# Kernel optimization log

Hardware: AMD Instinct MI355X
Metric: run time of the kernel (lower is better)

Reference implementation:

```python
import math
import jax, jax.numpy as jnp
import numpy as np

D_MODEL = 1024
N_HEAD = 16
HEAD_DIM = D_MODEL // N_HEAD
THETA = 10000.0


def precompute_rope(seq_len, head_dim):
    half = head_dim // 2
    inv_freq = 1.0 / (THETA ** (jnp.arange(half, dtype=jnp.float32) / half))
    pos = jnp.arange(seq_len, dtype=jnp.float32)
    freqs = jnp.outer(pos, inv_freq)  # [S, half]
    return jnp.cos(freqs), jnp.sin(freqs)


def apply_rope(x, cos, sin):
    # x: [B, H, S, Dh]; cos/sin: [S, Dh//2] -> broadcast over B, H
    x_even = x[..., 0::2]
    x_odd = x[..., 1::2]
    cos = cos[None, None]
    sin = sin[None, None]
    out_even = x_even * cos - x_odd * sin
    out_odd = x_even * sin + x_odd * cos
    # interleave back: stack on last axis then flatten pairs
    return jnp.stack((out_even, out_odd), axis=-1).reshape(x.shape)


def setup_inputs() -> dict:
    key = jax.random.key(0)
    kx, kq, kp = jax.random.split(key, 3)
    x = jax.random.normal(kx, (4, 2048, D_MODEL), dtype=jnp.float32)
    s = 1.0 / math.sqrt(D_MODEL)
    # torch Linear weight is [out, in]; we store transposed [in, out] for x @ W
    W_qkv = jax.random.normal(kq, (D_MODEL, 3 * D_MODEL), dtype=jnp.float32) * s
    W_proj = jax.random.normal(kp, (D_MODEL, D_MODEL), dtype=jnp.float32) * s
    return {"x": x, "W_qkv": W_qkv, "W_proj": W_proj}


def reference(x, W_qkv, W_proj):
    bsz, seqlen, d_model = x.shape
    qkv = x @ W_qkv  # [B, S, 3D]
    q, k, v = jnp.split(qkv, 3, axis=-1)
    def to_heads(t):
        return t.reshape(bsz, seqlen, N_HEAD, HEAD_DIM).transpose(0, 2, 1, 3)
    q, k, v = to_heads(q), to_heads(k), to_heads(v)  # [B, H, S, Dh]
    cos, sin = precompute_rope(seqlen, HEAD_DIM)
    q = apply_rope(q, cos, sin)
    k = apply_rope(k, cos, sin)
    att = jnp.einsum('bhqd,bhkd->bhqk', q, k) * (1.0 / math.sqrt(HEAD_DIM))
    causal = jnp.tril(jnp.ones((seqlen, seqlen), dtype=bool))
    att = jnp.where(causal[None, None], att, -jnp.inf)
    att = jax.nn.softmax(att, axis=-1)
    y = jnp.einsum('bhqk,bhkd->bhqd', att, v)
    y = y.transpose(0, 2, 1, 3).reshape(bsz, seqlen, d_model)
    return y @ W_proj
```

## Files before the change

### kernel.cpp

```cpp
#include <hip/hip_runtime.h>


#define BATCH 4
#define SEQ   2048
#define DM    1024
#define NH    16
#define HD    64
#define QKV_W 3072

typedef short bf16x8 __attribute__((ext_vector_type(8)));
typedef float f32x4  __attribute__((ext_vector_type(4)));
typedef unsigned short bf16_t;

__device__ __forceinline__ unsigned short f2bf(float f) {
  unsigned u = __float_as_uint(f);
  u += 0x7fffu + ((u >> 16) & 1u);
  return (unsigned short)(u >> 16);
}
__device__ __forceinline__ float bf2f(unsigned short s) {
  return __uint_as_float((unsigned)s << 16);
}
__device__ __forceinline__ void gld16(const void* g, void* l) {
  __builtin_amdgcn_global_load_lds(
      (const __attribute__((address_space(1))) unsigned int*)g,
      (__attribute__((address_space(3))) unsigned int*)l, 16, 0, 0);
}

__global__ __launch_bounds__(256) void k_transpose(const float* __restrict__ W,
                                                   bf16_t* __restrict__ Wt,
                                                   int K, int N) {
  __shared__ float tile[32][33];
  const int tx = threadIdx.x, ty = threadIdx.y;
  const int n0 = blockIdx.x * 32, k0 = blockIdx.y * 32;
#pragma unroll
  for (int j = 0; j < 4; ++j)
    tile[ty + j * 8][tx] = W[(size_t)(k0 + ty + j * 8) * N + n0 + tx];
  __syncthreads();
#pragma unroll
  for (int j = 0; j < 4; ++j)
    Wt[(size_t)(n0 + ty + j * 8) * K + k0 + tx] = f2bf(tile[tx][ty + j * 8]);
}

__global__ __launch_bounds__(256) void k_cvt(const float* __restrict__ x,
                                             bf16_t* __restrict__ xb) {
  const int i = (blockIdx.x * 256 + threadIdx.x) * 4;
  float4 v = *(const float4*)(x + i);
  unsigned lo = (unsigned)f2bf(v.x) | ((unsigned)f2bf(v.y) << 16);
  unsigned hi = (unsigned)f2bf(v.z) | ((unsigned)f2bf(v.w) << 16);
  *(uint2*)(xb + i) = make_uint2(lo, hi);
}

__global__ __launch_bounds__(256) void k_rope(bf16_t* __restrict__ qkv) {
  const int t = blockIdx.x * 256 + threadIdx.x;
  const int i = t & 31;
  const int h = (t >> 5) & 15;
  const int s = (t >> 9) & 2047;
  const int b = t >> 20;
  const float inv = __expf((float)i * -0.28782313662425575f);
  float sn, cs;
  sincosf((float)s * inv, &sn, &cs);
  size_t base = ((size_t)(b * SEQ + s)) * QKV_W + h * HD + 2 * i;
#pragma unroll
  for (int part = 0; part < 2; ++part) {
    unsigned u = *(unsigned*)(qkv + base + part * DM);
    float e = bf2f((unsigned short)(u & 0xffffu));
    float o = bf2f((unsigned short)(u >> 16));
    unsigned short e2 = f2bf(e * cs - o * sn);
    unsigned short o2 = f2bf(e * sn + o * cs);
    *(unsigned*)(qkv + base + part * DM) = (unsigned)e2 | ((unsigned)o2 << 16);
  }
}

template<int MODE>
__global__ __launch_bounds__(256) void k_gemm(const bf16_t* __restrict__ A,
                                              const bf16_t* __restrict__ Bt,
                                              void* __restrict__ Cout,
                                              bf16_t* __restrict__ vt,
                                              int M, int N, int K) {
  __shared__ __align__(16) short As[128 * 32];
  __shared__ __align__(16) short Bs[128 * 32];
  const int tid = threadIdx.x;
  const int wave = tid >> 6, lane = tid & 63;
  const int quad = lane >> 4, l16 = lane & 15;
  const int wm = (wave >> 1) * 64, wn = (wave & 1) * 64;
  const int bm = blockIdx.y * 128, bn = blockIdx.x * 128;

  f32x4 acc[4][4];
#pragma unroll
  for (int i = 0; i < 4; ++i)
#pragma unroll
    for (int j = 0; j < 4; ++j) acc[i][j] = f32x4{0.f, 0.f, 0.f, 0.f};

  const int r0 = tid >> 2;
  const int c0 = (tid & 3) * 8;
  const bf16_t* Ap  = A  + (size_t)(bm + r0) * K + c0;
  const bf16_t* Ap2 = Ap + (size_t)64 * K;
  const bf16_t* Bp  = Bt + (size_t)(bn + r0) * K + c0;
  const bf16_t* Bp2 = Bp + (size_t)64 * K;
  short* Ad  = As + tid * 8;
  short* Ad2 = As + (256 + tid) * 8;
  short* Bd  = Bs + tid * 8;
  short* Bd2 = Bs + (256 + tid) * 8;

  for (int k0 = 0; k0 < K; k0 += 32) {
    __syncthreads();
    gld16(Ap + k0,  Ad);
    gld16(Ap2 + k0, Ad2);
    gld16(Bp + k0,  Bd);
    gld16(Bp2 + k0, Bd2);
    __syncthreads();
    bf16x8 af[4], bfr[4];
#pragma unroll
    for (int i = 0; i < 4; ++i)
      af[i] = *(const bf16x8*)&As[(wm + i * 16 + l16) * 32 + quad * 8];
#pragma unroll
    for (int j = 0; j < 4; ++j)
      bfr[j] = *(const bf16x8*)&Bs[(wn + j * 16 + l16) * 32 + quad * 8];
#pragma unroll
    for (int i = 0; i < 4; ++i)
#pragma unroll
      for (int j = 0; j < 4; ++j)
        acc[i][j] = __builtin_amdgcn_mfma_f32_16x16x32_bf16(af[i], bfr[j], acc[i][j], 0, 0, 0);
  }
#pragma unroll
  for (int i = 0; i < 4; ++i)
#pragma unroll
    for (int j = 0; j < 4; ++j) {
      const int col = bn + wn + j * 16 + l16;
      const int row0 = bm + wm + i * 16 + quad * 4;
      if (MODE == 1 && col >= 2048) {
        const int d = col - 2048;
        const int hh = d >> 6, dd = d & 63;
        const int bb = row0 >> 11, ss = row0 & 2047;
        ushort4 pk;
        pk.x = f2bf(acc[i][j][0]); pk.y = f2bf(acc[i][j][1]);
        pk.z = f2bf(acc[i][j][2]); pk.w = f2bf(acc[i][j][3]);
        *(ushort4*)(vt + ((size_t)((bb * NH + hh) * HD + dd)) * SEQ + ss) = pk;
      } else {
#pragma unroll
        for (int r = 0; r < 4; ++r) {
          if (MODE == 1)
            ((bf16_t*)Cout)[(size_t)(row0 + r) * N + col] = f2bf(acc[i][j][r]);
          else
            ((float*)Cout)[(size_t)(row0 + r) * N + col] = acc[i][j][r];
        }
      }
    }
}

__global__ __launch_bounds__(256, 4) void k_attn(const bf16_t* __restrict__ qkv,
                                                 const bf16_t* __restrict__ vt,
                                                 bf16_t* __restrict__ y) {
  __shared__ __align__(16) short KV[2][4][64 * 32];
  __shared__ __align__(16) short Pb[4][16 * 64];
  const int tid = threadIdx.x;
  const int wave = tid >> 6, lane = tid & 63;
  const int quad = lane >> 4, l16 = lane & 15;
  const int l = blockIdx.x;
  const int p = (l >> 3) & 15;
  const int g = ((l >> 7) << 3) | (l & 7);
  const int h = g & 15, b = g >> 4;
  const size_t bbase = (size_t)b * SEQ * QKV_W;
  short* Pw = &Pb[wave][0];
  const int srow = tid >> 2;
  const int sc8  = (tid & 3) * 8;
  const bf16_t* kbase = qkv + bbase + (size_t)srow * QKV_W + DM + h * HD + sc8;
  const bf16_t* vbase = vt + ((size_t)(b * NH + h) * HD + srow) * SEQ + sc8;

#define ISSUE(kv0, buf)                                              \
  do {                                                               \
    gld16(kbase + (size_t)(kv0) * QKV_W,      &KV[buf][0][tid * 8]); \
    gld16(kbase + (size_t)(kv0) * QKV_W + 32, &KV[buf][1][tid * 8]); \
    gld16(vbase + (kv0),                      &KV[buf][2][tid * 8]); \
    gld16(vbase + (kv0) + 32,                 &KV[buf][3][tid * 8]); \
  } while (0)

  int bufp = 0;
  ISSUE(0, 0);
  for (int half = 0; half < 2; ++half) {
    const int qt = half ? (31 - p) : p;
    const int qrow0 = qt * 64 + wave * 16;
    bf16x8 aq0, aq1;
    {
      const bf16_t* qp = qkv + bbase + (size_t)(qrow0 + l16) * QKV_W + h * HD + quad * 8;
      aq0 = *(const bf16x8*)qp;
      aq1 = *(const bf16x8*)(qp + 32);
    }
    f32x4 o[4];
    float lsum[4];
#pragma unroll
    for (int jn = 0; jn < 4; ++jn) o[jn] = f32x4{0.f, 0.f, 0.f, 0.f};
#pragma unroll
    for (int r = 0; r < 4; ++r) lsum[r] = 0.f;

    for (int t = 0; t <= qt; ++t) {
      const int kv0 = t * 64;
      __syncthreads();
      if (t < qt)            ISSUE(kv0 + 64, bufp ^ 1);
      else if (half == 0)    ISSUE(0, bufp ^ 1);
      const short* Kc0 = &KV[bufp][0][0];
      const short* Kc1 = &KV[bufp][1][0];
      const short* Vc0 = &KV[bufp][2][0];
      const short* Vc1 = &KV[bufp][3][0];

      f32x4 sacc[4];
#pragma unroll
      for (int jn = 0; jn < 4; ++jn) {
        bf16x8 bk0 = *(const bf16x8*)&Kc0[(jn * 16 + l16) * 32 + quad * 8];
        bf16x8 bk1 = *(const bf16x8*)&Kc1[(jn * 16 + l16) * 32 + quad * 8];
        f32x4 s4 = f32x4{0.f, 0.f, 0.f, 0.f};
        s4 = __builtin_amdgcn_mfma_f32_16x16x32_bf16(aq0, bk0, s4, 0, 0, 0);
        s4 = __builtin_amdgcn_mfma_f32_16x16x32_bf16(aq1, bk1, s4, 0, 0, 0);
        sacc[jn] = s4;
      }
      if (t == qt) {
#pragma unroll
        for (int r = 0; r < 4; ++r) {
          const int prow = quad * 4 + r;
          const int qr = qrow0 + prow;
#pragma unroll
          for (int jn = 0; jn < 4; ++jn) {
            const int kvcol = kv0 + jn * 16 + l16;
            float e = (kvcol <= qr) ? __expf(sacc[jn][r] * 0.125f - 8.0f) : 0.f;
            lsum[r] += e;
            const int pcol = jn * 16 + l16;
            Pw[prow * 64 + ((((pcol >> 3) ^ (prow & 7))) << 3) + (pcol & 7)] =
                (short)(__float_as_uint(e) >> 16);
          }
        }
      } else {
#pragma unroll
        for (int r = 0; r < 4; ++r) {
          const int prow = quad * 4 + r;
#pragma unroll
          for (int jn = 0; jn < 4; ++jn) {
            float e = __expf(sacc[jn][r] * 0.125f - 8.0f);
            lsum[r] += e;
            const int pcol = jn * 16 + l16;
            Pw[prow * 64 + ((((pcol >> 3) ^ (prow & 7))) << 3) + (pcol & 7)] =
                (short)(__float_as_uint(e) >> 16);
          }
        }
      }
#pragma unroll
      for (int ks = 0; ks < 2; ++ks) {
        bf16x8 ap = *(const bf16x8*)&Pw[l16 * 64 + (((ks * 4 + quad) ^ (l16 & 7)) << 3)];
        const short* Vc = ks ? Vc1 : Vc0;
#pragma unroll
        for (int jn = 0; jn < 4; ++jn) {
          bf16x8 bv = *(const bf16x8*)&Vc[(jn * 16 + l16) * 32 + quad * 8];
          o[jn] = __builtin_amdgcn_mfma_f32_16x16x32_bf16(ap, bv, o[jn], 0, 0, 0);
        }
      }
      bufp ^= 1;
    }
#pragma unroll
    for (int r = 0; r < 4; ++r) {
      float s = lsum[r];
      s += __shfl_xor(s, 1, 64);
      s += __shfl_xor(s, 2, 64);
      s += __shfl_xor(s, 4, 64);
      s += __shfl_xor(s, 8, 64);
      const float invl = 1.0f / s;
      const int qr = qrow0 + quad * 4 + r;
      bf16_t* yp = y + ((size_t)b * SEQ + qr) * DM + h * HD;
#pragma unroll
      for (int jn = 0; jn < 4; ++jn)
        yp[jn * 16 + l16] = f2bf(o[jn][r] * invl);
    }
  }
#undef ISSUE
}

extern "C" void kernel_launch(void* const* d_in, const int* in_sizes, int n_in,
                              void* d_out, int out_size, void* d_ws, size_t ws_size,
                              hipStream_t stream) {
  const float* x     = (const float*)d_in[0];
  const float* Wqkv  = (const float*)d_in[1];
  const float* Wproj = (const float*)d_in[2];
  float* out = (float*)d_out;
  char* ws = (char*)d_ws;
  bf16_t* qkv = (bf16_t*)(ws);
  bf16_t* Wt1 = (bf16_t*)(ws + 50331648);
  bf16_t* Wt2 = (bf16_t*)(ws + 56623104);
  bf16_t* xb  = (bf16_t*)(ws + 58720256);
  bf16_t* y   = xb;
  bf16_t* vt  = (bf16_t*)d_out;

  k_transpose<<<dim3(QKV_W / 32, DM / 32), dim3(32, 8), 0, stream>>>(Wqkv, Wt1, DM, QKV_W);
  k_transpose<<<dim3(DM / 32, DM / 32), dim3(32, 8), 0, stream>>>(Wproj, Wt2, DM, DM);
  k_cvt<<<(BATCH * SEQ * DM) / (4 * 256), 256, 0, stream>>>(x, xb);
  k_gemm<1><<<dim3(QKV_W / 128, (BATCH * SEQ) / 128), 256, 0, stream>>>(
      xb, Wt1, qkv, vt, BATCH * SEQ, QKV_W, DM);
  k_rope<<<(BATCH * SEQ * NH * 32) / 256, 256, 0, stream>>>(qkv);
  k_attn<<<1024, 256, 0, stream>>>(qkv, vt, y);
  k_gemm<0><<<dim3(DM / 128, (BATCH * SEQ) / 128), 256, 0, stream>>>(
      y, Wt2, out, nullptr, BATCH * SEQ, DM, DM);
}
```

Measured before the change: 279.5 us.

## Double attention query tile per wave and widen GEMM K-tile with swizzled LDS

The attention kernel now gives each block a 128-row query tile, with each wave owning 32 rows, so every K/V tile loaded into LDS feeds twice as many MFMAs. The grid is halved to 512 blocks and the occupancy hint drops to 2 blocks per CU. Q is prescaled by log2(e)/sqrt(d) so the softmax can use exp2 directly, and fully visible tiles skip the causal mask. The GEMM moves to a 64-wide K step with XOR-swizzled LDS, which halves the number of barrier pairs and is meant to reduce bank conflicts. In exchange, register pressure rises, there are fewer blocks, and the causal diagonal leaves some waves idle on partially masked tiles.

```diff
diff --git a/kernel.cpp b/kernel.cpp
--- a/kernel.cpp
+++ b/kernel.cpp
@@ -77,8 +77,8 @@
                                               void* __restrict__ Cout,
                                               bf16_t* __restrict__ vt,
                                               int M, int N, int K) {
-  __shared__ __align__(16) short As[128 * 32];
-  __shared__ __align__(16) short Bs[128 * 32];
+  __shared__ __align__(16) short As[128 * 64];
+  __shared__ __align__(16) short Bs[128 * 64];
   const int tid = threadIdx.x;
   const int wave = tid >> 6, lane = tid & 63;
   const int quad = lane >> 4, l16 = lane & 15;
@@ -91,36 +91,38 @@
 #pragma unroll
     for (int j = 0; j < 4; ++j) acc[i][j] = f32x4{0.f, 0.f, 0.f, 0.f};
 
-  const int r0 = tid >> 2;
-  const int c0 = (tid & 3) * 8;
-  const bf16_t* Ap  = A  + (size_t)(bm + r0) * K + c0;
-  const bf16_t* Ap2 = Ap + (size_t)64 * K;
-  const bf16_t* Bp  = Bt + (size_t)(bn + r0) * K + c0;
-  const bf16_t* Bp2 = Bp + (size_t)64 * K;
-  short* Ad  = As + tid * 8;
-  short* Ad2 = As + (256 + tid) * 8;
-  short* Bd  = Bs + tid * 8;
-  short* Bd2 = Bs + (256 + tid) * 8;
-
-  for (int k0 = 0; k0 < K; k0 += 32) {
+  const int srow = tid >> 3;
+  const int sg   = (tid & 7) ^ (srow & 7);
+  const bf16_t* Ap = A  + (size_t)(bm + srow) * K + sg * 8;
+  const bf16_t* Bp = Bt + (size_t)(bn + srow) * K + sg * 8;
+  short* Ad = As + tid * 8;
+  short* Bd = Bs + tid * 8;
+
+  for (int k0 = 0; k0 < K; k0 += 64) {
     __syncthreads();
-    gld16(Ap + k0,  Ad);
-    gld16(Ap2 + k0, Ad2);
-    gld16(Bp + k0,  Bd);
-    gld16(Bp2 + k0, Bd2);
+#pragma unroll
+    for (int pp = 0; pp < 4; ++pp) {
+      gld16(Ap + (size_t)(pp * 32) * K + k0, Ad + pp * 2048);
+      gld16(Bp + (size_t)(pp * 32) * K + k0, Bd + pp * 2048);
+    }
     __syncthreads();
-    bf16x8 af[4], bfr[4];
-#pragma unroll
-    for (int i = 0; i < 4; ++i)
-      af[i] = *(const bf16x8*)&As[(wm + i * 16 + l16) * 32 + quad * 8];
-#pragma unroll
-    for (int j = 0; j < 4; ++j)
-      bfr[j] = *(const bf16x8*)&Bs[(wn + j * 16 + l16) * 32 + quad * 8];
-#pragma unroll
-    for (int i = 0; i < 4; ++i)
+#pragma unroll
+    for (int ks = 0; ks < 2; ++ks) {
+      bf16x8 af[4], bfr[4];
+#pragma unroll
+      for (int i = 0; i < 4; ++i)
+        af[i] = *(const bf16x8*)&As[(wm + i * 16 + l16) * 64 +
+                                    (((ks * 4 + quad) ^ (l16 & 7)) << 3)];
 #pragma unroll
       for (int j = 0; j < 4; ++j)
-        acc[i][j] = __builtin_amdgcn_mfma_f32_16x16x32_bf16(af[i], bfr[j], acc[i][j], 0, 0, 0);
+        bfr[j] = *(const bf16x8*)&Bs[(wn + j * 16 + l16) * 64 +
+                                     (((ks * 4 + quad) ^ (l16 & 7)) << 3)];
+#pragma unroll
+      for (int i = 0; i < 4; ++i)
+#pragma unroll
+        for (int j = 0; j < 4; ++j)
+          acc[i][j] = __builtin_amdgcn_mfma_f32_16x16x32_bf16(af[i], bfr[j], acc[i][j], 0, 0, 0);
+    }
   }
 #pragma unroll
   for (int i = 0; i < 4; ++i)
@@ -148,17 +150,18 @@
     }
 }
 
-__global__ __launch_bounds__(256, 4) void k_attn(const bf16_t* __restrict__ qkv,
+#define QSCALE 0.18033688011112042f
+__global__ __launch_bounds__(256, 2) void k_attn(const bf16_t* __restrict__ qkv,
                                                  const bf16_t* __restrict__ vt,
                                                  bf16_t* __restrict__ y) {
   __shared__ __align__(16) short KV[2][4][64 * 32];
-  __shared__ __align__(16) short Pb[4][16 * 64];
+  __shared__ __align__(16) short Pb[4][32 * 64];
   const int tid = threadIdx.x;
   const int wave = tid >> 6, lane = tid & 63;
   const int quad = lane >> 4, l16 = lane & 15;
   const int l = blockIdx.x;
-  const int p = (l >> 3) & 15;
-  const int g = ((l >> 7) << 3) | (l & 7);
+  const int p = (l >> 3) & 7;
+  const int g = ((l >> 6) << 3) | (l & 7);
   const int h = g & 15, b = g >> 4;
   const size_t bbase = (size_t)b * SEQ * QKV_W;
   short* Pw = &Pb[wave][0];
@@ -178,96 +181,107 @@
   int bufp = 0;
   ISSUE(0, 0);
   for (int half = 0; half < 2; ++half) {
-    const int qt = half ? (31 - p) : p;
-    const int qrow0 = qt * 64 + wave * 16;
-    bf16x8 aq0, aq1;
-    {
-      const bf16_t* qp = qkv + bbase + (size_t)(qrow0 + l16) * QKV_W + h * HD + quad * 8;
-      aq0 = *(const bf16x8*)qp;
-      aq1 = *(const bf16x8*)(qp + 32);
-    }
-    f32x4 o[4];
-    float lsum[4];
-#pragma unroll
-    for (int jn = 0; jn < 4; ++jn) o[jn] = f32x4{0.f, 0.f, 0.f, 0.f};
-#pragma unroll
-    for (int r = 0; r < 4; ++r) lsum[r] = 0.f;
-
-    for (int t = 0; t <= qt; ++t) {
-      const int kv0 = t * 64;
+    const int qt = half ? (15 - p) : p;
+    const int qb = qt * 128 + wave * 32;
+    bf16x8 aq[2][2];
+#pragma unroll
+    for (int mi = 0; mi < 2; ++mi)
+#pragma unroll
+      for (int kk = 0; kk < 2; ++kk) {
+        const bf16_t* qp = qkv + bbase + (size_t)(qb + mi * 16 + l16) * QKV_W +
+                           h * HD + kk * 32 + quad * 8;
+        bf16x8 raw = *(const bf16x8*)qp;
+        bf16x8 sc;
+#pragma unroll
+        for (int e = 0; e < 8; ++e)
+          sc[e] = (short)f2bf(bf2f((unsigned short)raw[e]) * QSCALE);
+        aq[mi][kk] = sc;
+      }
+    f32x4 o[2][4];
+    float lsum[2][4];
+#pragma unroll
+    for (int mi = 0; mi < 2; ++mi)
+#pragma unroll
+      for (int jn = 0; jn < 4; ++jn) o[mi][jn] = f32x4{0.f, 0.f, 0.f, 0.f};
+#pragma unroll
+    for (int mi = 0; mi < 2; ++mi)
+#pragma unroll
+      for (int r = 0; r < 4; ++r) lsum[mi][r] = 0.f;
+
+    const int jmax = 2 * qt + 1;
+    for (int j = 0; j <= jmax; ++j) {
+      const int kv0 = j * 64;
       __syncthreads();
-      if (t < qt)            ISSUE(kv0 + 64, bufp ^ 1);
+      if (j < jmax)          ISSUE(kv0 + 64, bufp ^ 1);
       else if (half == 0)    ISSUE(0, bufp ^ 1);
-      const short* Kc0 = &KV[bufp][0][0];
-      const short* Kc1 = &KV[bufp][1][0];
-      const short* Vc0 = &KV[bufp][2][0];
-      const short* Vc1 = &KV[bufp][3][0];
-
-      f32x4 sacc[4];
-#pragma unroll
-      for (int jn = 0; jn < 4; ++jn) {
-        bf16x8 bk0 = *(const bf16x8*)&Kc0[(jn * 16 + l16) * 32 + quad * 8];
-        bf16x8 bk1 = *(const bf16x8*)&Kc1[(jn * 16 + l16) * 32 + quad * 8];
-        f32x4 s4 = f32x4{0.f, 0.f, 0.f, 0.f};
-        s4 = __builtin_amdgcn_mfma_f32_16x16x32_bf16(aq0, bk0, s4, 0, 0, 0);
-        s4 = __builtin_amdgcn_mfma_f32_16x16x32_bf16(aq1, bk1, s4, 0, 0, 0);
-        sacc[jn] = s4;
-      }
-      if (t == qt) {
-#pragma unroll
-        for (int r = 0; r < 4; ++r) {
-          const int prow = quad * 4 + r;
-          const int qr = qrow0 + prow;
-#pragma unroll
-          for (int jn = 0; jn < 4; ++jn) {
-            const int kvcol = kv0 + jn * 16 + l16;
-            float e = (kvcol <= qr) ? __expf(sacc[jn][r] * 0.125f - 8.0f) : 0.f;
-            lsum[r] += e;
-            const int pcol = jn * 16 + l16;
-            Pw[prow * 64 + ((((pcol >> 3) ^ (prow & 7))) << 3) + (pcol & 7)] =
-                (short)(__float_as_uint(e) >> 16);
+      if (kv0 <= qb + 31) {
+        const bool needmask = (kv0 + 63 > qb);
+        const short* Kc0 = &KV[bufp][0][0];
+        const short* Kc1 = &KV[bufp][1][0];
+        const short* Vc0 = &KV[bufp][2][0];
+        const short* Vc1 = &KV[bufp][3][0];
+
+        f32x4 sacc[2][4];
+#pragma unroll
+        for (int jn = 0; jn < 4; ++jn) {
+          bf16x8 bk0 = *(const bf16x8*)&Kc0[(jn * 16 + l16) * 32 + quad * 8];
+          bf16x8 bk1 = *(const bf16x8*)&Kc1[(jn * 16 + l16) * 32 + quad * 8];
+#pragma unroll
+          for (int mi = 0; mi < 2; ++mi) {
+            f32x4 s4 = f32x4{0.f, 0.f, 0.f, 0.f};
+            s4 = __builtin_amdgcn_mfma_f32_16x16x32_bf16(aq[mi][0], bk0, s4, 0, 0, 0);
+            s4 = __builtin_amdgcn_mfma_f32_16x16x32_bf16(aq[mi][1], bk1, s4, 0, 0, 0);
+            sacc[mi][jn] = s4;
           }
         }
-      } else {
-#pragma unroll
-        for (int r = 0; r < 4; ++r) {
-          const int prow = quad * 4 + r;
+#pragma unroll
+        for (int mi = 0; mi < 2; ++mi)
+#pragma unroll
+          for (int r = 0; r < 4; ++r) {
+            const int prow = mi * 16 + quad * 4 + r;
+            const int qr = qb + prow;
+#pragma unroll
+            for (int jn = 0; jn < 4; ++jn) {
+              float e = __builtin_amdgcn_exp2f(sacc[mi][jn][r]);
+              if (needmask) e = (kv0 + jn * 16 + l16 <= qr) ? e : 0.f;
+              lsum[mi][r] += e;
+              const int pcol = jn * 16 + l16;
+              Pw[prow * 64 + ((((pcol >> 3) ^ (prow & 7))) << 3) + (pcol & 7)] =
+                  (short)(__float_as_uint(e) >> 16);
+            }
+          }
+#pragma unroll
+        for (int ks = 0; ks < 2; ++ks) {
+          const int gsw = ((ks * 4 + quad) ^ (l16 & 7)) << 3;
+          bf16x8 ap0 = *(const bf16x8*)&Pw[l16 * 64 + gsw];
+          bf16x8 ap1 = *(const bf16x8*)&Pw[(16 + l16) * 64 + gsw];
+          const short* Vc = ks ? Vc1 : Vc0;
 #pragma unroll
           for (int jn = 0; jn < 4; ++jn) {
-            float e = __expf(sacc[jn][r] * 0.125f - 8.0f);
-            lsum[r] += e;
-            const int pcol = jn * 16 + l16;
-            Pw[prow * 64 + ((((pcol >> 3) ^ (prow & 7))) << 3) + (pcol & 7)] =
-                (short)(__float_as_uint(e) >> 16);
+            bf16x8 bv = *(const bf16x8*)&Vc[(jn * 16 + l16) * 32 + quad * 8];
+            o[0][jn] = __builtin_amdgcn_mfma_f32_16x16x32_bf16(ap0, bv, o[0][jn], 0, 0, 0);
+            o[1][jn] = __builtin_amdgcn_mfma_f32_16x16x32_bf16(ap1, bv, o[1][jn], 0, 0, 0);
           }
-        }
-      }
-#pragma unroll
-      for (int ks = 0; ks < 2; ++ks) {
-        bf16x8 ap = *(const bf16x8*)&Pw[l16 * 64 + (((ks * 4 + quad) ^ (l16 & 7)) << 3)];
-        const short* Vc = ks ? Vc1 : Vc0;
-#pragma unroll
-        for (int jn = 0; jn < 4; ++jn) {
-          bf16x8 bv = *(const bf16x8*)&Vc[(jn * 16 + l16) * 32 + quad * 8];
-          o[jn] = __builtin_amdgcn_mfma_f32_16x16x32_bf16(ap, bv, o[jn], 0, 0, 0);
         }
       }
       bufp ^= 1;
     }
 #pragma unroll
-    for (int r = 0; r < 4; ++r) {
-      float s = lsum[r];
-      s += __shfl_xor(s, 1, 64);
-      s += __shfl_xor(s, 2, 64);
-      s += __shfl_xor(s, 4, 64);
-      s += __shfl_xor(s, 8, 64);
-      const float invl = 1.0f / s;
-      const int qr = qrow0 + quad * 4 + r;
-      bf16_t* yp = y + ((size_t)b * SEQ + qr) * DM + h * HD;
-#pragma unroll
-      for (int jn = 0; jn < 4; ++jn)
-        yp[jn * 16 + l16] = f2bf(o[jn][r] * invl);
-    }
+    for (int mi = 0; mi < 2; ++mi)
+#pragma unroll
+      for (int r = 0; r < 4; ++r) {
+        float s = lsum[mi][r];
+        s += __shfl_xor(s, 1, 64);
+        s += __shfl_xor(s, 2, 64);
+        s += __shfl_xor(s, 4, 64);
+        s += __shfl_xor(s, 8, 64);
+        const float invl = 1.0f / s;
+        const int qr = qb + mi * 16 + quad * 4 + r;
+        bf16_t* yp = y + ((size_t)b * SEQ + qr) * DM + h * HD;
+#pragma unroll
+        for (int jn = 0; jn < 4; ++jn)
+          yp[jn * 16 + l16] = f2bf(o[mi][jn][r] * invl);
+      }
   }
 #undef ISSUE
 }
@@ -293,7 +307,7 @@
   k_gemm<1><<<dim3(QKV_W / 128, (BATCH * SEQ) / 128), 256, 0, stream>>>(
       xb, Wt1, qkv, vt, BATCH * SEQ, QKV_W, DM);
   k_rope<<<(BATCH * SEQ * NH * 32) / 256, 256, 0, stream>>>(qkv);
-  k_attn<<<1024, 256, 0, stream>>>(qkv, vt, y);
+  k_attn<<<512, 256, 0, stream>>>(qkv, vt, y);
   k_gemm<0><<<dim3(DM / 128, (BATCH * SEQ) / 128), 256, 0, stream>>>(
       y, Wt2, out, nullptr, BATCH * SEQ, DM, DM);
 }
```

After: 264.6 us. -5.3%, faster.
